# Performance work log

Hardware: AMD Instinct MI355X
Metric: run time of the kernel (lower is better)

Reference implementation:

```python
import jax, jax.numpy as jnp
import numpy as np

TOK = 256        # flattened batch*seq tokens (decode-style, memory-bound)
IN_F = 4096
OUT_F = 4096
N_OUTLIER = 32


def quantize_rowwise(x):
    """Symmetric rowwise int8 quantization: scale = rowwise absmax."""
    scale = jnp.max(jnp.abs(x), axis=-1)                      # [rows]
    safe = jnp.maximum(scale, 1e-8)
    q = jnp.clip(jnp.round(x / safe[:, None] * 127.0), -127.0, 127.0)
    return q, scale


def setup_inputs() -> dict:
    key = jax.random.key(0)
    k1, k2, k3, k4, k5 = jax.random.split(key, 5)
    x = jax.random.normal(k1, (TOK, IN_F), jnp.float32)
    weight_int8 = jax.random.randint(k2, (OUT_F, IN_F), -127, 128, jnp.int32)
    weight_scales = jax.random.uniform(k3, (OUT_F,), jnp.float32, minval=0.5, maxval=2.0)
    # spread unique outlier column indices across in_features
    outlier_indices = jnp.arange(N_OUTLIER, dtype=jnp.int32) * (IN_F // N_OUTLIER)
    outlier_weights = jax.random.normal(k4, (OUT_F, N_OUTLIER), jnp.float32) * 0.02
    bias = jax.random.normal(k5, (OUT_F,), jnp.float32) * 0.01
    # from_linear zeros outlier columns of the int8 weight before quantization
    weight_int8 = weight_int8.at[:, outlier_indices].set(0)
    return {"x": x, "weight_int8": weight_int8, "weight_scales": weight_scales,
            "outlier_indices": outlier_indices, "outlier_weights": outlier_weights,
            "bias": bias}


def reference(x, weight_int8, weight_scales, outlier_indices, outlier_weights, bias):
    # _forward_mixed: outlier columns handled in fp, rest quantize->dequant int8.
    # Selecting the non-outlier columns is equivalent to zeroing the outlier
    # columns (the dropped weight columns contribute 0 to the GEMM, and the
    # rowwise absmax scale is unaffected since |0| = 0). This keeps shapes
    # static and jit-friendly while computing identical math.
    in_f = x.shape[-1]
    mask = jnp.ones((in_f,), dtype=bool).at[outlier_indices].set(False)

    x_main = x * mask                                         # [T, in]
    xq, xs = quantize_rowwise(x_main)                         # int8-valued fp, [T]
    x_fp = xq * (xs[:, None] / 127.0)                         # dequantized activations

    w_fp = (weight_int8 * mask).astype(jnp.float32) * (weight_scales[:, None] / 127.0)  # [out, in]
    out_main = x_fp @ w_fp.T                                  # [T, out]

    x_outlier = x[:, outlier_indices]                         # [T, n_out]
    out_outlier = x_outlier @ outlier_weights.T               # [T, out]

    return out_main + out_outlier + bias
```

## Files before the change

### kernel.cpp

```cpp
#include <hip/hip_runtime.h>
#include <stdint.h>

#define TOK 256
#define IN_F 4096
#define OUT_F 4096
#define N_OUT 32

typedef int v4i  __attribute__((ext_vector_type(4)));
typedef int v16i __attribute__((ext_vector_type(16)));

__device__ __forceinline__ void gll16(const void* g, void* l) {
    __builtin_amdgcn_global_load_lds((const __attribute__((address_space(1))) void*)g,
                                     (__attribute__((address_space(3))) void*)l, 16, 0, 0);
}

__global__ __launch_bounds__(256) void oal_quant(
    const float* __restrict__ x, const int* __restrict__ oidx,
    int8_t* __restrict__ xqt, float* __restrict__ xs, float* __restrict__ xo)
{
    const int row = blockIdx.x;
    const int tid = threadIdx.x;
    __shared__ unsigned char flags[IN_F];
    __shared__ float wmax[4];
    __shared__ float s_scale;

    const float* xr = x + (size_t)row * IN_F;
    float4 v[4];
    const float4* xp = reinterpret_cast<const float4*>(xr + tid * 16);
    #pragma unroll
    for (int i = 0; i < 4; ++i) v[i] = xp[i];

    *reinterpret_cast<uint4*>(&flags[tid * 16]) = make_uint4(0u, 0u, 0u, 0u);
    __syncthreads();
    if (tid < N_OUT) flags[oidx[tid]] = 1;
    __syncthreads();

    uint4 f = *reinterpret_cast<const uint4*>(&flags[tid * 16]);
    unsigned int fw[4] = { f.x, f.y, f.z, f.w };
    float vals[16];
    #pragma unroll
    for (int i = 0; i < 4; ++i) {
        vals[i*4+0] = ((fw[i]      ) & 255u) ? 0.0f : v[i].x;
        vals[i*4+1] = ((fw[i] >>  8) & 255u) ? 0.0f : v[i].y;
        vals[i*4+2] = ((fw[i] >> 16) & 255u) ? 0.0f : v[i].z;
        vals[i*4+3] = ((fw[i] >> 24) & 255u) ? 0.0f : v[i].w;
    }

    float m = 0.0f;
    #pragma unroll
    for (int i = 0; i < 16; ++i) m = fmaxf(m, fabsf(vals[i]));
    #pragma unroll
    for (int off = 32; off > 0; off >>= 1) m = fmaxf(m, __shfl_xor(m, off, 64));
    const int lane = tid & 63, wid = tid >> 6;
    if (lane == 0) wmax[wid] = m;
    __syncthreads();
    if (tid == 0) {
        float s = fmaxf(fmaxf(wmax[0], wmax[1]), fmaxf(wmax[2], wmax[3]));
        s_scale = s;
        xs[row] = s;
    }
    __syncthreads();
    const float safe = fmaxf(s_scale, 1e-8f);

    int q[16];
    #pragma unroll
    for (int i = 0; i < 16; ++i) {
        float t = vals[i] / safe * 127.0f;
        t = fminf(127.0f, fmaxf(-127.0f, rintf(t)));
        q[i] = (int)t;
    }
    uint4 packed;
    unsigned int* pw = &packed.x;
    #pragma unroll
    for (int i = 0; i < 4; ++i)
        pw[i] = (unsigned)(q[i*4] & 255) | ((unsigned)(q[i*4+1] & 255) << 8)
              | ((unsigned)(q[i*4+2] & 255) << 16) | ((unsigned)(q[i*4+3] & 255) << 24);

    const int ks32  = tid >> 1;
    const int khalf = tid & 1;
    const int rowgrp = row >> 5;
    *reinterpret_cast<uint4*>(xqt + (size_t)ks32 * 8192 + rowgrp * 1024
                              + (khalf * 32 + (row & 31)) * 16) = packed;

    if (tid < N_OUT) xo[row * N_OUT + tid] = xr[oidx[tid]];
}

template<int MODE>
__global__ __launch_bounds__(512, 1) void oal_gemm(
    const int8_t* __restrict__ xqt, const int* __restrict__ wgt,
    int* __restrict__ pout)
{
    __shared__ __align__(16) int8_t sm[131072];
    int8_t* As = sm;
    int8_t* Bs = sm + 65536;

    const int bn = blockIdx.x;
    const int ntile = bn & 31, kslice = bn >> 5;
    const int n0 = ntile * 128;
    const int tid = threadIdx.x, lane = tid & 63, wv = tid >> 6;
    const int mg = wv & 3, ng = wv >> 2;
    const int l31 = lane & 31, lh = lane >> 5;

    auto issueA = [&](int h) {
        const int8_t* s = xqt + ((size_t)(kslice * 16 + h * 4) << 13) + tid * 16;
        int8_t* d = As + ((h & 1) << 15) + tid * 16;
        gll16(s, d);
        gll16(s + 8192, d + 8192);
        gll16(s + 16384, d + 16384);
        gll16(s + 24576, d + 24576);
    };
    issueA(0);

    {
        const int cbase = wv * 16;
        #pragma unroll
        for (int g = 0; g < 4; ++g) {
            int4 t[8];
            #pragma unroll
            for (int j = 0; j < 8; ++j) {
                const int q = g * 8 + j;
                const int c = cbase + (q & 15);
                const int ih = q >> 4;
                t[j] = *reinterpret_cast<const int4*>(
                    wgt + (size_t)(n0 + c) * IN_F + kslice * 512 + ih * 256 + lane * 4);
            }
            #pragma unroll
            for (int j = 0; j < 8; ++j) {
                const int q = g * 8 + j;
                const int c = cbase + (q & 15);
                const int ih = q >> 4;
                unsigned pk = (unsigned)((t[j].x & 255) | ((t[j].y & 255) << 8)
                             | ((t[j].z & 255) << 16) | ((t[j].w & 255) << 24));
                const int ks32l = ih * 8 + (lane >> 3);
                const int addr = ks32l * 4096 + (c >> 5) * 1024
                               + (((lane >> 2) & 1) * 32 + ((c & 31) ^ (lane >> 3))) * 16
                               + (lane & 3) * 4;
                *reinterpret_cast<unsigned*>(Bs + addr) = pk;
            }
        }
    }
    __syncthreads();

    v16i acc00 = {}, acc01 = {}, acc10 = {}, acc11 = {};
    const int aoff = (2 * mg) * 1024 + lane * 16;
    #pragma unroll
    for (int h = 0; h < 4; ++h) {
        if (h < 3) issueA(h + 1);
        const int8_t* At = As + ((h & 1) << 15);
        #pragma unroll
        for (int loc = 0; loc < 4; ++loc) {
            const int ks32g = h * 4 + loc;
            const int s7 = ks32g & 7;
            const int8_t* Ap = At + loc * 8192 + aoff;
            const int8_t* Bp = Bs + ks32g * 4096 + (lh * 32 + (l31 ^ s7)) * 16;
            v4i a0 = *reinterpret_cast<const v4i*>(Ap);
            v4i a1 = *reinterpret_cast<const v4i*>(Ap + 1024);
            v4i b0 = *reinterpret_cast<const v4i*>(Bp + (2 * ng) * 1024);
            v4i b1 = *reinterpret_cast<const v4i*>(Bp + (2 * ng + 1) * 1024);
            acc00 = __builtin_amdgcn_mfma_i32_32x32x32_i8(a0, b0, acc00, 0, 0, 0);
            acc01 = __builtin_amdgcn_mfma_i32_32x32x32_i8(a0, b1, acc01, 0, 0, 0);
            acc10 = __builtin_amdgcn_mfma_i32_32x32x32_i8(a1, b0, acc10, 0, 0, 0);
            acc11 = __builtin_amdgcn_mfma_i32_32x32x32_i8(a1, b1, acc11, 0, 0, 0);
        }
        if (h < 3) __syncthreads();
    }

    const int colb = n0 + ng * 64 + l31;
    const int rowb = mg * 64 + 4 * lh;
#define OUTW(ACC, MF, NF) { _Pragma("unroll") \
    for (int r = 0; r < 16; ++r) { \
        const int rr = rowb + (MF)*32 + (r & 3) + ((r >> 2) << 3); \
        const size_t off = (size_t)rr * OUT_F + colb + (NF)*32; \
        if (MODE == 0) pout[(size_t)kslice * ((size_t)TOK * OUT_F) + off] = ACC[r]; \
        else atomicAdd(pout + off, ACC[r]); \
    } }
    OUTW(acc00,0,0) OUTW(acc01,0,1) OUTW(acc10,1,0) OUTW(acc11,1,1)
#undef OUTW
}

template<int MODE>
__global__ __launch_bounds__(256) void oal_epi(
    float* __restrict__ outp, const int* __restrict__ part,
    const float* __restrict__ xs, const float* __restrict__ wscale,
    const float* __restrict__ ow, const float* __restrict__ bias,
    const float* __restrict__ xo)
{
    const int rb = blockIdx.x >> 3;
    const int cb = blockIdx.x & 7;
    const int tid = threadIdx.x;
    const int c0 = cb * 512 + tid * 2;

    __shared__ float sxo[8][32];
    __shared__ float sxs[8];
    if (tid < 64) {
        const int rr = tid >> 3, jj = tid & 7;
        *reinterpret_cast<float4*>(&sxo[rr][jj * 4]) =
            *reinterpret_cast<const float4*>(xo + (size_t)(rb * 8 + rr) * N_OUT + jj * 4);
    }
    if (tid < 8) sxs[tid] = xs[rb * 8 + tid];
    __syncthreads();

    float o0[32], o1[32];
    #pragma unroll
    for (int j = 0; j < 8; ++j) {
        float4 f0 = reinterpret_cast<const float4*>(ow + (size_t)c0 * N_OUT)[j];
        float4 f1 = reinterpret_cast<const float4*>(ow + (size_t)(c0 + 1) * N_OUT)[j];
        o0[j*4+0]=f0.x; o0[j*4+1]=f0.y; o0[j*4+2]=f0.z; o0[j*4+3]=f0.w;
        o1[j*4+0]=f1.x; o1[j*4+1]=f1.y; o1[j*4+2]=f1.z; o1[j*4+3]=f1.w;
    }
    const float wsc0 = wscale[c0]     * (1.0f / 16129.0f);
    const float wsc1 = wscale[c0 + 1] * (1.0f / 16129.0f);
    const float bo0 = bias[c0], bo1 = bias[c0 + 1];

    #pragma unroll
    for (int r = 0; r < 8; ++r) {
        const int row = rb * 8 + r;
        const size_t off = (size_t)row * OUT_F + c0;
        int px = 0, py = 0;
        if (MODE == 0) {
            #pragma unroll
            for (int s2 = 0; s2 < 8; ++s2) {
                int2 t = *reinterpret_cast<const int2*>(
                    part + (size_t)s2 * ((size_t)TOK * OUT_F) + off);
                px += t.x; py += t.y;
            }
        } else {
            int2 t = *reinterpret_cast<const int2*>(reinterpret_cast<const int*>(outp) + off);
            px = t.x; py = t.y;
        }
        float d0 = 0.f, d1 = 0.f;
        #pragma unroll
        for (int k = 0; k < 32; ++k) {
            const float xv = sxo[r][k];
            d0 += xv * o0[k]; d1 += xv * o1[k];
        }
        const float s = sxs[r];
        float2 res;
        res.x = (float)px * (s * wsc0) + d0 + bo0;
        res.y = (float)py * (s * wsc1) + d1 + bo1;
        *reinterpret_cast<float2*>(outp + off) = res;
    }
}

extern "C" void kernel_launch(void* const* d_in, const int* in_sizes, int n_in,
                              void* d_out, int out_size, void* d_ws, size_t ws_size,
                              hipStream_t stream) {
    const float* x      = (const float*)d_in[0];
    const int*   w      = (const int*)  d_in[1];
    const float* wscale = (const float*)d_in[2];
    const int*   oidx   = (const int*)  d_in[3];
    const float* ow     = (const float*)d_in[4];
    const float* bias   = (const float*)d_in[5];
    float* out = (float*)d_out;

    int8_t* xqt = (int8_t*)d_ws;
    float*  xs  = (float*)((char*)d_ws + (1 << 20));
    float*  xo  = (float*)((char*)d_ws + (1 << 20) + 1024);
    int*    P2  = (int*)  ((char*)d_ws + (1 << 20) + 1024 + 32768);
    const size_t need = (size_t)(1 << 20) + 1024 + 32768 + (size_t)8 * TOK * OUT_F * 4;

    oal_quant<<<TOK, 256, 0, stream>>>(x, oidx, xqt, xs, xo);
    if (ws_size >= need) {
        oal_gemm<0><<<256, 512, 0, stream>>>(xqt, w, P2);
        oal_epi<0><<<256, 256, 0, stream>>>(out, P2, xs, wscale, ow, bias, xo);
    } else {
        hipMemsetAsync(d_out, 0, (size_t)TOK * OUT_F * 4, stream);
        oal_gemm<1><<<256, 512, 0, stream>>>(xqt, w, (int*)d_out);
        oal_epi<1><<<256, 256, 0, stream>>>(out, (const int*)d_out, xs, wscale, ow, bias, xo);
    }
}
```

Baseline: 122.8 us.

## Split activation quantization into absmax pass and tiled LDS-transposed quant kernel

The fused per-row quantize kernel, which wrote 16-byte chunks scattered into the GEMM's interleaved xqt layout, becomes two kernels. One computes the row absmax and gathers the outlier values. The other reloads x in 32-row by 128-column tiles, quantizes them, and transposes through a swizzled LDS buffer so xqt is written in contiguous 1KB runs. This is meant to make the xqt writes coalesced, at the cost of an extra kernel launch and a second read of x (4MB).

Measured after the change: 124.1 us. Within noise of the previous version (+1.1%).

```diff
diff --git a/kernel.cpp b/kernel.cpp
--- a/kernel.cpp
+++ b/kernel.cpp
@@ -14,15 +14,14 @@
                                      (__attribute__((address_space(3))) void*)l, 16, 0, 0);
 }
 
-__global__ __launch_bounds__(256) void oal_quant(
+__global__ __launch_bounds__(256) void oal_absmax(
     const float* __restrict__ x, const int* __restrict__ oidx,
-    int8_t* __restrict__ xqt, float* __restrict__ xs, float* __restrict__ xo)
+    float* __restrict__ xs, float* __restrict__ xo)
 {
     const int row = blockIdx.x;
     const int tid = threadIdx.x;
     __shared__ unsigned char flags[IN_F];
     __shared__ float wmax[4];
-    __shared__ float s_scale;
 
     const float* xr = x + (size_t)row * IN_F;
     float4 v[4];
@@ -37,52 +36,78 @@
 
     uint4 f = *reinterpret_cast<const uint4*>(&flags[tid * 16]);
     unsigned int fw[4] = { f.x, f.y, f.z, f.w };
-    float vals[16];
+    float m = 0.0f;
     #pragma unroll
     for (int i = 0; i < 4; ++i) {
-        vals[i*4+0] = ((fw[i]      ) & 255u) ? 0.0f : v[i].x;
-        vals[i*4+1] = ((fw[i] >>  8) & 255u) ? 0.0f : v[i].y;
-        vals[i*4+2] = ((fw[i] >> 16) & 255u) ? 0.0f : v[i].z;
-        vals[i*4+3] = ((fw[i] >> 24) & 255u) ? 0.0f : v[i].w;
-    }
-
-    float m = 0.0f;
-    #pragma unroll
-    for (int i = 0; i < 16; ++i) m = fmaxf(m, fabsf(vals[i]));
+        float a0 = ((fw[i]      ) & 255u) ? 0.0f : v[i].x;
+        float a1 = ((fw[i] >>  8) & 255u) ? 0.0f : v[i].y;
+        float a2 = ((fw[i] >> 16) & 255u) ? 0.0f : v[i].z;
+        float a3 = ((fw[i] >> 24) & 255u) ? 0.0f : v[i].w;
+        m = fmaxf(m, fmaxf(fmaxf(fabsf(a0), fabsf(a1)), fmaxf(fabsf(a2), fabsf(a3))));
+    }
     #pragma unroll
     for (int off = 32; off > 0; off >>= 1) m = fmaxf(m, __shfl_xor(m, off, 64));
     const int lane = tid & 63, wid = tid >> 6;
     if (lane == 0) wmax[wid] = m;
     __syncthreads();
-    if (tid == 0) {
-        float s = fmaxf(fmaxf(wmax[0], wmax[1]), fmaxf(wmax[2], wmax[3]));
-        s_scale = s;
-        xs[row] = s;
-    }
-    __syncthreads();
-    const float safe = fmaxf(s_scale, 1e-8f);
-
-    int q[16];
-    #pragma unroll
-    for (int i = 0; i < 16; ++i) {
-        float t = vals[i] / safe * 127.0f;
-        t = fminf(127.0f, fmaxf(-127.0f, rintf(t)));
-        q[i] = (int)t;
-    }
-    uint4 packed;
-    unsigned int* pw = &packed.x;
-    #pragma unroll
-    for (int i = 0; i < 4; ++i)
-        pw[i] = (unsigned)(q[i*4] & 255) | ((unsigned)(q[i*4+1] & 255) << 8)
-              | ((unsigned)(q[i*4+2] & 255) << 16) | ((unsigned)(q[i*4+3] & 255) << 24);
-
-    const int ks32  = tid >> 1;
-    const int khalf = tid & 1;
-    const int rowgrp = row >> 5;
-    *reinterpret_cast<uint4*>(xqt + (size_t)ks32 * 8192 + rowgrp * 1024
-                              + (khalf * 32 + (row & 31)) * 16) = packed;
+    if (tid == 0)
+        xs[row] = fmaxf(fmaxf(wmax[0], wmax[1]), fmaxf(wmax[2], wmax[3]));
 
     if (tid < N_OUT) xo[row * N_OUT + tid] = xr[oidx[tid]];
+}
+
+__global__ __launch_bounds__(256) void oal_qtile(
+    const float* __restrict__ x, const int* __restrict__ oidx,
+    const float* __restrict__ xs, int8_t* __restrict__ xqt)
+{
+    const int rg  = blockIdx.x >> 5;
+    const int ksl = blockIdx.x & 31;
+    const int tid = threadIdx.x;
+    __shared__ unsigned char fl[128];
+    __shared__ __align__(16) int8_t T[32 * 128];
+
+    if (tid < 128) fl[tid] = 0;
+    __syncthreads();
+    if (tid < N_OUT) {
+        const int ix = oidx[tid];
+        if ((ix >> 7) == ksl) fl[ix & 127] = 1;
+    }
+    __syncthreads();
+
+    const int row_l = tid >> 3, kc = tid & 7;
+    const int row = rg * 32 + row_l;
+    const float safe = fmaxf(xs[row], 1e-8f);
+    const float4* src = reinterpret_cast<const float4*>(
+        x + (size_t)row * IN_F + ksl * 128 + kc * 16);
+    float4 v[4];
+    #pragma unroll
+    for (int i = 0; i < 4; ++i) v[i] = src[i];
+
+    const float* vv = reinterpret_cast<const float*>(v);
+    unsigned pk[4];
+    #pragma unroll
+    for (int wds = 0; wds < 4; ++wds) {
+        int q[4];
+        #pragma unroll
+        for (int j = 0; j < 4; ++j) {
+            const int i = wds * 4 + j;
+            const float val = fl[kc * 16 + i] ? 0.0f : vv[i];
+            float t = val / safe * 127.0f;
+            t = fminf(127.0f, fmaxf(-127.0f, rintf(t)));
+            q[j] = (int)t;
+        }
+        pk[wds] = (unsigned)((q[0] & 255) | ((q[1] & 255) << 8)
+                 | ((q[2] & 255) << 16) | ((q[3] & 255) << 24));
+    }
+    *reinterpret_cast<uint4*>(&T[row_l * 128 + ((kc ^ (row_l & 7)) * 16)]) =
+        make_uint4(pk[0], pk[1], pk[2], pk[3]);
+    __syncthreads();
+
+    const int tile = tid >> 6, a = tid & 63;
+    const int rr = a & 31;
+    const int chunk = tile * 2 + (a >> 5);
+    uint4 val = *reinterpret_cast<const uint4*>(&T[rr * 128 + ((chunk ^ (rr & 7)) * 16)]);
+    *reinterpret_cast<uint4*>(xqt + (size_t)(ksl * 4 + tile) * 8192 + rg * 1024 + a * 16) = val;
 }
 
 template<int MODE>
@@ -259,7 +284,8 @@
     int*    P2  = (int*)  ((char*)d_ws + (1 << 20) + 1024 + 32768);
     const size_t need = (size_t)(1 << 20) + 1024 + 32768 + (size_t)8 * TOK * OUT_F * 4;
 
-    oal_quant<<<TOK, 256, 0, stream>>>(x, oidx, xqt, xs, xo);
+    oal_absmax<<<TOK, 256, 0, stream>>>(x, oidx, xs, xo);
+    oal_qtile<<<256, 256, 0, stream>>>(x, oidx, xs, xqt);
     if (ws_size >= need) {
         oal_gemm<0><<<256, 512, 0, stream>>>(xqt, w, P2);
         oal_epi<0><<<256, 256, 0, stream>>>(out, P2, xs, wscale, ow, bias, xo);
```
